# Performance work log

Hardware: AMD Instinct MI355X
Metric: run time of the kernel (lower is better)

## Reference

```python
import jax, jax.numpy as jnp
import numpy as np
import math

B, S, H, DM = 1, 2048, 16, 1024
DK = DM // H
MAX_SEQ = 2048  # rel_embed has MAX_SEQ+1 rows


def setup_inputs() -> dict:
    rng = jax.random.key(0)
    ks = jax.random.split(rng, 12)
    w = lambda k, shape, s=0.02: (jax.random.normal(k, shape, jnp.float32) * s)
    inp = {
        'query': jax.random.normal(ks[0], (B, S, DM), jnp.float32),
        'key':   jax.random.normal(ks[1], (B, S, DM), jnp.float32),
        'value': jax.random.normal(ks[2], (B, S, DM), jnp.float32),
        # causal integer mask [B,S,S] (cumsum over it derives rel-pos indices)
        'mask': jnp.broadcast_to(jnp.tril(jnp.ones((S, S), jnp.int32)), (B, S, S)),
        'Wq': w(ks[3], (DM, DM)), 'bq': jnp.zeros((DM,), jnp.float32),
        'Wk': w(ks[4], (DM, DM)), 'bk': jnp.zeros((DM,), jnp.float32),
        'Wv': w(ks[5], (DM, DM)), 'bv': jnp.zeros((DM,), jnp.float32),
        'Wo': w(ks[6], (DM, DM)), 'bo': jnp.zeros((DM,), jnp.float32),
        # relative position embeddings [h, max_seq_len+1, d_k], N(0,1) as in the module
        'rel_embed': jax.random.normal(ks[7], (H, MAX_SEQ + 1, DK), jnp.float32),
    }
    return inp


def reference(query, key, value, mask, Wq, bq, Wk, bk, Wv, bv, Wo, bo, rel_embed):
    scale = 1.0 / math.sqrt(DK)
    heads = lambda x, W, b: (x @ W.T + b).reshape(B, S, H, DK).transpose(0, 2, 1, 3)
    q = heads(query, Wq, bq)   # [B,H,S,DK]
    k = heads(key, Wk, bk)
    v = heads(value, Wv, bv)

    scores = jnp.einsum('bhid,bhjd->bhij', q, k) * scale  # [B,H,S,S]

    m4 = mask[:, None, :, :]                 # [B,1,S,S]
    nz = m4 != 0
    # torch: cumsum(mask)-1 picks the m-index; index 0 (then zeroed) where mask==0
    m_idx = jnp.where(nz, jnp.cumsum(m4, axis=-1) - 1, 0)  # [B,1,S,S]

    # rel_scores[b,h,m,l] = <q[b,h,l,:], rel_embed[h,m,:]> / sqrt(d_k)
    rel = jnp.einsum('bhld,hmd->bhml', q, rel_embed[:, :S]) * scale  # [B,H,S,S]
    idx = jnp.broadcast_to(m_idx, (B, H, S, S))
    # torch.take flat-index decodes to rel[b,h, m_idx[i,j], j]
    rel_g = jnp.take_along_axis(rel, idx, axis=2) * nz.astype(scores.dtype)

    scores = jnp.where(nz, scores + rel_g, jnp.float32(-1e9))
    p = jax.nn.softmax(scores, axis=-1)      # dropout p=0.0 -> identity

    out = jnp.einsum('bhij,bhjd->bhid', p, v)         # [B,H,S,DK]
    out = out.transpose(0, 2, 1, 3).reshape(B, S, DM)  # [B,S,DM]
    return out @ Wo.T + bo
```

## Files before the change

### kernel.cpp

```cpp
#include <hip/hip_runtime.h>

typedef __bf16 bf16_t;
typedef __bf16 bf16x4 __attribute__((ext_vector_type(4)));
typedef __bf16 bf16x8 __attribute__((ext_vector_type(8)));
typedef float  f32x4  __attribute__((ext_vector_type(4)));
typedef float  f32x16 __attribute__((ext_vector_type(16)));
typedef unsigned int u32;

#define S_LEN 2048
#define DMODEL 1024
#define NHEAD 16
#define DHEAD 64
#define RELROWS 2049

__device__ __forceinline__ void gload16(const void* g, void* l) {
    __builtin_amdgcn_global_load_lds((const __attribute__((address_space(1))) void*)g,
                                     (__attribute__((address_space(3))) void*)l,
                                     16, 0, 0);
}

__device__ __forceinline__ f32x4 mfma16(bf16x8 a, bf16x8 b, f32x4 c) {
    return __builtin_amdgcn_mfma_f32_16x16x32_bf16(a, b, c, 0, 0, 0);
}
__device__ __forceinline__ f32x16 mfma32(bf16x8 a, bf16x8 b, f32x16 c) {
    return __builtin_amdgcn_mfma_f32_32x32x16_bf16(a, b, c, 0, 0, 0);
}

__device__ __forceinline__ bf16x8 lds_read_swz(const bf16_t* base, int row, int colb) {
    return *(const bf16x8*)((const char*)base + row * 128 + (colb ^ ((row & 7) << 4)));
}

__device__ __forceinline__ u32 cvtpk(float lo, float hi) {
    u32 w;
    asm("v_cvt_pk_bf16_f32 %0, %1, %2" : "=v"(w) : "v"(lo), "v"(hi));
    return w;
}
__device__ __forceinline__ void swap32(u32& a, u32& b) {
    asm("v_permlane32_swap_b32 %0, %1" : "+v"(a), "+v"(b));
}
__device__ __forceinline__ float fexp2(float x) {
    float r;
    asm("v_exp_f32 %0, %1" : "=v"(r) : "v"(x));
    return r;
}

__global__ __launch_bounds__(256)
void f2bf_all(const float* __restrict__ xq, const float* __restrict__ xk,
              const float* __restrict__ xv,
              const float* __restrict__ wq, const float* __restrict__ wk,
              const float* __restrict__ wv, const float* __restrict__ wo,
              bf16_t* __restrict__ dst, int n4X, int n4W) {
    const int i = blockIdx.x * blockDim.x + threadIdx.x;
    const float* src; int j;
    if (i < 3 * n4X) {
        if (i < n4X)            { src = xq; j = i; }
        else if (i < 2 * n4X)   { src = xk; j = i - n4X; }
        else                    { src = xv; j = i - 2 * n4X; }
    } else {
        int w = i - 3 * n4X;
        if (w < n4W)            { src = wq; j = w; }
        else if (w < 2 * n4W)   { src = wk; j = w - n4W; }
        else if (w < 3 * n4W)   { src = wv; j = w - 2 * n4W; }
        else                    { src = wo; j = w - 3 * n4W; }
    }
    float4 v = ((const float4*)src)[j];
    bf16x4 o;
    o[0] = (bf16_t)v.x; o[1] = (bf16_t)v.y; o[2] = (bf16_t)v.z; o[3] = (bf16_t)v.w;
    ((bf16x4*)dst)[i] = o;
}

template <int BM, int BN>
__global__ __launch_bounds__(256)
void gemm_qkv(const bf16_t* __restrict__ Abase, const bf16_t* __restrict__ Wbase,
              const float* __restrict__ b0, const float* __restrict__ b1,
              const float* __restrict__ b2,
              bf16_t* __restrict__ outb,
              const float* __restrict__ relp, float* __restrict__ RGout,
              bf16_t* __restrict__ vtp,
              int M, int N, int K) {
    __shared__ alignas(16) bf16_t As[2][BM * 64];
    __shared__ alignas(16) bf16_t Bs[2][BN * 64];
    const int tid = threadIdx.x, lane = tid & 63, wave = tid >> 6;
    const int z = blockIdx.z;
    const bf16_t* A = Abase + (size_t)z * M * K;
    const bf16_t* W = Wbase + (size_t)z * N * K;
    const float* bias = (z == 0) ? b0 : (z == 1 ? b1 : b2);
    const int nwg = gridDim.x * gridDim.y;
    const int wg = blockIdx.y * gridDim.x + blockIdx.x;
    const int swz = (wg & 7) * (nwg >> 3) + (wg >> 3);
    const int m0 = (swz / gridDim.x) * BM, n0 = (swz % gridDim.x) * BN;
    const int wr = (wave >> 1) * (BM / 2), wc = (wave & 1) * (BN / 2);
    constexpr int MR = BM / 32, NR = BN / 32;
    constexpr int LOADS = BM / 32 + BN / 32;

    f32x4 acc[MR][NR] = {};
    const int soff = wave * 1024 + lane * 16;

    auto stage = [&](int b, int kt) {
#pragma unroll
        for (int r = 0; r < BM / 32; ++r) {
            int L = r * 4096 + soff;
            int row = L >> 7, colb = (L & 127) ^ ((row & 7) << 4);
            gload16(A + (size_t)(m0 + row) * K + kt + (colb >> 1),
                    (char*)As[b] + r * 4096 + wave * 1024);
        }
#pragma unroll
        for (int r = 0; r < BN / 32; ++r) {
            int L = r * 4096 + soff;
            int row = L >> 7, colb = (L & 127) ^ ((row & 7) << 4);
            gload16(W + (size_t)(n0 + row) * K + kt + (colb >> 1),
                    (char*)Bs[b] + r * 4096 + wave * 1024);
        }
    };

    const int NK = K >> 6;
    stage(0, 0);
    for (int s = 0; s < NK; ++s) {
        const int buf = s & 1;
        if (s + 1 < NK) {
            stage(buf ^ 1, (s + 1) << 6);
            if constexpr (LOADS == 6) asm volatile("s_waitcnt vmcnt(6)" ::: "memory");
            else if constexpr (LOADS == 4) asm volatile("s_waitcnt vmcnt(4)" ::: "memory");
            else asm volatile("s_waitcnt vmcnt(8)" ::: "memory");
        } else {
            asm volatile("s_waitcnt vmcnt(0)" ::: "memory");
        }
        asm volatile("s_barrier" ::: "memory");
#pragma unroll
        for (int kk = 0; kk < 2; ++kk) {
            bf16x8 af[MR], bfr[NR];
#pragma unroll
            for (int m = 0; m < MR; ++m)
                af[m] = lds_read_swz(As[buf], wr + m * 16 + (lane & 15),
                                     kk * 64 + (lane >> 4) * 16);
#pragma unroll
            for (int n = 0; n < NR; ++n)
                bfr[n] = lds_read_swz(Bs[buf], wc + n * 16 + (lane & 15),
                                      kk * 64 + (lane >> 4) * 16);
#pragma unroll
            for (int m = 0; m < MR; ++m)
#pragma unroll
                for (int n = 0; n < NR; ++n)
                    acc[m][n] = mfma16(af[m], bfr[n], acc[m][n]);
        }
        asm volatile("s_barrier" ::: "memory");
    }

    const float scale = (z == 0) ? 0.18033688011112042f : 1.0f;
    float rp[MR][4];
#pragma unroll
    for (int m = 0; m < MR; ++m)
#pragma unroll
        for (int r2 = 0; r2 < 4; ++r2) rp[m][r2] = 0.f;
    const int hh = n0 >> 6;
#pragma unroll
    for (int m = 0; m < MR; ++m) {
        const int gi = m0 + wr + m * 16 + (lane >> 4) * 4;
#pragma unroll
        for (int n = 0; n < NR; ++n) {
            const int gj = n0 + wc + n * 16 + (lane & 15);
            const float bv = bias[gj];
            if (z == 2) {
                bf16x4 o4;
#pragma unroll
                for (int r2 = 0; r2 < 4; ++r2) o4[r2] = (bf16_t)(acc[m][n][r2] + bv);
                *(bf16x4*)&vtp[(size_t)gj * S_LEN + gi] = o4;
            } else {
#pragma unroll
                for (int r2 = 0; r2 < 4; ++r2) {
                    float v = (acc[m][n][r2] + bv) * scale;
                    outb[(size_t)z * M * N + (size_t)(gi + r2) * N + gj] = (bf16_t)v;
                    if (z == 0)
                        rp[m][r2] += v * relp[((size_t)hh * RELROWS + (gi + r2)) * DHEAD + (gj & 63)];
                }
            }
        }
    }
    if (z == 0) {
        constexpr int HM = BM / 2;
        float* Rp = (float*)As;
#pragma unroll
        for (int m = 0; m < MR; ++m)
#pragma unroll
            for (int r2 = 0; r2 < 4; ++r2) {
                float p = rp[m][r2];
                p += __shfl_xor(p, 1);
                p += __shfl_xor(p, 2);
                p += __shfl_xor(p, 4);
                p += __shfl_xor(p, 8);
                if ((lane & 15) == 0)
                    Rp[wave * HM + m * 16 + (lane >> 4) * 4 + r2] = p;
            }
        __syncthreads();
        if ((wave & 1) == 0) {
#pragma unroll
            for (int rr0 = 0; rr0 < HM; rr0 += 64) {
                int rr = rr0 + lane;
                float v = Rp[wave * HM + rr] + Rp[(wave + 1) * HM + rr];
                RGout[hh * S_LEN + m0 + wr + rr] = v;
            }
        }
    }
}

__global__ __launch_bounds__(256)
void gemm_out(const bf16_t* __restrict__ A, const bf16_t* __restrict__ W,
              const float* __restrict__ bias, float* __restrict__ outf,
              int M, int N, int K) {
    __shared__ alignas(16) bf16_t As[4][64 * 64];
    __shared__ alignas(16) bf16_t Bs[4][64 * 64];
    const int tid = threadIdx.x, lane = tid & 63, wave = tid >> 6;
    const int nwg = gridDim.x * gridDim.y;
    const int wg = blockIdx.y * gridDim.x + blockIdx.x;
    const int swz = (wg & 7) * (nwg >> 3) + (wg >> 3);
    const int m0 = (swz / gridDim.x) * 64, n0 = (swz % gridDim.x) * 64;
    const int wr = (wave >> 1) * 32, wc = (wave & 1) * 32;

    f32x4 acc[2][2] = {};
    const int soff = wave * 1024 + lane * 16;

    auto stage = [&](int b, int kt) {
#pragma unroll
        for (int r = 0; r < 2; ++r) {
            int L = r * 4096 + soff;
            int row = L >> 7, colb = (L & 127) ^ ((row & 7) << 4);
            gload16(A + (size_t)(m0 + row) * K + kt + (colb >> 1),
                    (char*)As[b] + r * 4096 + wave * 1024);
        }
#pragma unroll
        for (int r = 0; r < 2; ++r) {
            int L = r * 4096 + soff;
            int row = L >> 7, colb = (L & 127) ^ ((row & 7) << 4);
            gload16(W + (size_t)(n0 + row) * K + kt + (colb >> 1),
                    (char*)Bs[b] + r * 4096 + wave * 1024);
        }
    };

    const int NK = K >> 6;
    stage(0, 0); stage(1, 64); stage(2, 128);
    for (int s = 0; s < NK; ++s) {
        if (s + 2 < NK)      asm volatile("s_waitcnt vmcnt(8)" ::: "memory");
        else if (s + 1 < NK) asm volatile("s_waitcnt vmcnt(4)" ::: "memory");
        else                 asm volatile("s_waitcnt vmcnt(0)" ::: "memory");
        asm volatile("s_barrier" ::: "memory");
        if (s + 3 < NK) stage((s + 3) & 3, (s + 3) << 6);
        const int buf = s & 3;
#pragma unroll
        for (int kk = 0; kk < 2; ++kk) {
            bf16x8 af[2], bfr[2];
#pragma unroll
            for (int m = 0; m < 2; ++m)
                af[m] = lds_read_swz(As[buf], wr + m * 16 + (lane & 15),
                                     kk * 64 + (lane >> 4) * 16);
#pragma unroll
            for (int n = 0; n < 2; ++n)
                bfr[n] = lds_read_swz(Bs[buf], wc + n * 16 + (lane & 15),
                                      kk * 64 + (lane >> 4) * 16);
#pragma unroll
            for (int m = 0; m < 2; ++m)
#pragma unroll
                for (int n = 0; n < 2; ++n)
                    acc[m][n] = mfma16(af[m], bfr[n], acc[m][n]);
        }
    }
#pragma unroll
    for (int m = 0; m < 2; ++m) {
        const int gi = m0 + wr + m * 16 + (lane >> 4) * 4;
#pragma unroll
        for (int n = 0; n < 2; ++n) {
            const int gj = n0 + wc + n * 16 + (lane & 15);
            const float bv = bias[gj];
#pragma unroll
            for (int r2 = 0; r2 < 4; ++r2)
                outf[(size_t)(gi + r2) * N + gj] = acc[m][n][r2] + bv;
        }
    }
}

__global__ __launch_bounds__(256, 2)
void flash_attn(const bf16_t* __restrict__ Qb, const bf16_t* __restrict__ Kb,
                const bf16_t* __restrict__ Vtp, const float* __restrict__ RG,
                bf16_t* __restrict__ Ob) {
    __shared__ alignas(16) bf16_t KB[4][64 * 64];
    __shared__ alignas(16) bf16_t VB[4][64 * 64];
    __shared__ alignas(16) float Rs[S_LEN];
    const int tid = threadIdx.x, lane = tid & 63, wave = tid >> 6;
    const int h = blockIdx.x;
    const int qt = (int)gridDim.y - 1 - (int)blockIdx.y;
    const int q0 = qt * 32;
    const int nt = (qt >> 1) + 1;
    const int qpar = qt & 1;
    const int lo5 = lane & 31, hi = lane >> 5;

    const int nkv = nt * 64;
    for (int i = tid * 8; i < nkv; i += 2048) {
        *(float4*)&Rs[i]     = *(const float4*)&RG[h * S_LEN + i];
        *(float4*)&Rs[i + 4] = *(const float4*)&RG[h * S_LEN + i + 4];
    }

    const bf16_t* qp = Qb + (size_t)(q0 + lo5) * DMODEL + h * DHEAD;
    bf16x8 qf[4];
#pragma unroll
    for (int c = 0; c < 4; ++c)
        qf[c] = *(const bf16x8*)(qp + c * 16 + hi * 8);

    auto stageK = [&](int tt) {
        char* dst = (char*)KB[wave];
#pragma unroll
        for (int rr = 0; rr < 8; ++rr) {
            int L = rr * 1024 + lane * 16;
            int row = L >> 7, colb = (L & 127) ^ ((row & 7) << 4);
            gload16(Kb + (size_t)(tt * 64 + row) * DMODEL + h * DHEAD + (colb >> 1),
                    dst + rr * 1024);
        }
    };
    auto stageV = [&](int tt) {
        char* dst = (char*)VB[wave];
#pragma unroll
        for (int rr = 0; rr < 8; ++rr) {
            int L = rr * 1024 + lane * 16;
            int row = L >> 7, colb = (L & 127) ^ ((row & 7) << 4);
            gload16(Vtp + (size_t)(h * DHEAD + row) * S_LEN + tt * 64 + (colb >> 1),
                    dst + rr * 1024);
        }
    };

    if (wave < nt) { stageK(wave); stageV(wave); }
    __syncthreads();

    f32x16 oacc[2] = {};
    float ls = 0.f;
    const int thr = qpar * 32 + lo5;

    for (int tt = wave; tt < nt; tt += 4) {
        const int kv0 = tt * 64;
        const bool diag = (tt == nt - 1);
        asm volatile("s_waitcnt vmcnt(8)" ::: "memory");

        f32x16 sta, stb;
#pragma unroll
        for (int g = 0; g < 4; ++g) {
            f32x4 ra = *(const f32x4*)&Rs[kv0 + g * 8 + hi * 4];
            f32x4 rb = *(const f32x4*)&Rs[kv0 + 32 + g * 8 + hi * 4];
#pragma unroll
            for (int e = 0; e < 4; ++e) { sta[g * 4 + e] = ra[e]; stb[g * 4 + e] = rb[e]; }
        }
        __builtin_amdgcn_s_setprio(1);
#pragma unroll
        for (int c = 0; c < 4; ++c) {
            bf16x8 kfa = lds_read_swz(KB[wave], lo5, c * 32 + hi * 16);
            sta = mfma32(kfa, qf[c], sta);
        }
#pragma unroll
        for (int c = 0; c < 4; ++c) {
            bf16x8 kfb = lds_read_swz(KB[wave], 32 + lo5, c * 32 + hi * 16);
            stb = mfma32(kfb, qf[c], stb);
        }
        __builtin_amdgcn_s_setprio(0);
        if (tt + 4 < nt) stageK(tt + 4);

        float pra[16], prb[16];
        if (diag) {
#pragma unroll
            for (int r = 0; r < 16; ++r) {
                int kloc = (r & 3) + 8 * (r >> 2) + 4 * hi;
                float va = fexp2(sta[r]), vb = fexp2(stb[r]);
                pra[r] = (kloc > thr) ? 0.f : va;
                prb[r] = (kloc + 32 > thr) ? 0.f : vb;
            }
        } else {
#pragma unroll
            for (int r = 0; r < 16; ++r) { pra[r] = fexp2(sta[r]); prb[r] = fexp2(stb[r]); }
        }
#pragma unroll
        for (int r = 0; r < 16; ++r) ls += pra[r] + prb[r];
        u32 pw[4][4];
#pragma unroll
        for (int hf = 0; hf < 2; ++hf) {
            u32 a  = cvtpk(pra[8 * hf + 0], pra[8 * hf + 1]);
            u32 b  = cvtpk(pra[8 * hf + 4], pra[8 * hf + 5]);
            swap32(a, b);
            u32 c2 = cvtpk(pra[8 * hf + 2], pra[8 * hf + 3]);
            u32 d2 = cvtpk(pra[8 * hf + 6], pra[8 * hf + 7]);
            swap32(c2, d2);
            pw[hf][0] = a;  pw[hf][1] = c2;  pw[hf][2] = b;  pw[hf][3] = d2;
        }
#pragma unroll
        for (int hf = 0; hf < 2; ++hf) {
            u32 a  = cvtpk(prb[8 * hf + 0], prb[8 * hf + 1]);
            u32 b  = cvtpk(prb[8 * hf + 4], prb[8 * hf + 5]);
            swap32(a, b);
            u32 c2 = cvtpk(prb[8 * hf + 2], prb[8 * hf + 3]);
            u32 d2 = cvtpk(prb[8 * hf + 6], prb[8 * hf + 7]);
            swap32(c2, d2);
            pw[2 + hf][0] = a;  pw[2 + hf][1] = c2;  pw[2 + hf][2] = b;  pw[2 + hf][3] = d2;
        }

        if (tt + 4 < nt) asm volatile("s_waitcnt vmcnt(8)" ::: "memory");
        else             asm volatile("s_waitcnt vmcnt(0)" ::: "memory");

        __builtin_amdgcn_s_setprio(1);
#pragma unroll
        for (int kc = 0; kc < 4; ++kc) {
            union { u32 w[4]; bf16x8 v; } uu;
            uu.w[0] = pw[kc][0]; uu.w[1] = pw[kc][1]; uu.w[2] = pw[kc][2]; uu.w[3] = pw[kc][3];
#pragma unroll
            for (int db = 0; db < 2; ++db) {
                bf16x8 vf = lds_read_swz(VB[wave], db * 32 + lo5, kc * 32 + hi * 16);
                oacc[db] = mfma32(vf, uu.v, oacc[db]);
            }
        }
        __builtin_amdgcn_s_setprio(0);
        if (tt + 4 < nt) stageV(tt + 4);
    }

    asm volatile("s_waitcnt vmcnt(0)" ::: "memory");
    __syncthreads();
    float* scr = (float*)KB;
    if (wave > 0) {
        float* base = scr + (wave - 1) * 2112 + lane * 32;
#pragma unroll
        for (int db = 0; db < 2; ++db)
#pragma unroll
            for (int g = 0; g < 4; ++g) {
                f32x4 v4;
#pragma unroll
                for (int e = 0; e < 4; ++e) v4[e] = oacc[db][g * 4 + e];
                *(f32x4*)(base + db * 16 + g * 4) = v4;
            }
        scr[(wave - 1) * 2112 + 2048 + lane] = ls;
    }
    __syncthreads();
    if (wave == 0) {
#pragma unroll
        for (int w2 = 0; w2 < 3; ++w2) {
            const float* base = scr + w2 * 2112 + lane * 32;
#pragma unroll
            for (int db = 0; db < 2; ++db)
#pragma unroll
                for (int g = 0; g < 4; ++g) {
                    f32x4 v4 = *(const f32x4*)(base + db * 16 + g * 4);
#pragma unroll
                    for (int e = 0; e < 4; ++e) oacc[db][g * 4 + e] += v4[e];
                }
            ls += scr[w2 * 2112 + 2048 + lane];
        }
        ls += __shfl_xor(ls, 32);
        const float inv = 1.0f / ls;
        const int qg = q0 + lo5;
#pragma unroll
        for (int db = 0; db < 2; ++db)
#pragma unroll
            for (int g = 0; g < 4; ++g) {
                bf16x4 o4;
#pragma unroll
                for (int e = 0; e < 4; ++e)
                    o4[e] = (bf16_t)(oacc[db][g * 4 + e] * inv);
                *(bf16x4*)&Ob[(size_t)qg * DMODEL + h * DHEAD + db * 32 + g * 8 + hi * 4] = o4;
            }
    }
}

extern "C" void kernel_launch(void* const* d_in, const int* in_sizes, int n_in,
                              void* d_out, int out_size, void* d_ws, size_t ws_size,
                              hipStream_t stream) {
    const float* query = (const float*)d_in[0];
    const float* key   = (const float*)d_in[1];
    const float* value = (const float*)d_in[2];
    const float* Wq  = (const float*)d_in[4];
    const float* bq  = (const float*)d_in[5];
    const float* Wk  = (const float*)d_in[6];
    const float* bk  = (const float*)d_in[7];
    const float* Wv  = (const float*)d_in[8];
    const float* bv  = (const float*)d_in[9];
    const float* Wo  = (const float*)d_in[10];
    const float* bo  = (const float*)d_in[11];
    const float* rel = (const float*)d_in[12];

    char* ws = (char*)d_ws;
    const size_t nX = (size_t)S_LEN * DMODEL;
    const size_t nW = (size_t)DMODEL * DMODEL;
    bf16_t* Xbf  = (bf16_t*)ws;
    bf16_t* Wbf  = (bf16_t*)(ws + 3 * nX * 2);
    bf16_t* QKV  = (bf16_t*)(ws + 3 * nX * 2 + 4 * nW * 2);
    float*  RG   = (float*)(ws + 3 * nX * 2 + 4 * nW * 2 + 3 * nX * 2);
    bf16_t* Vtp  = QKV + 2 * nX;
    bf16_t* AOb  = (bf16_t*)(ws + nX * 2);
    (void)in_sizes; (void)n_in; (void)out_size; (void)ws_size;

    const int n4X = (int)(nX / 4), n4W = (int)(nW / 4);
    const int tot4 = 3 * n4X + 4 * n4W;
    f2bf_all<<<tot4 / 256, 256, 0, stream>>>(query, key, value, Wq, Wk, Wv, Wo,
                                             Xbf, n4X, n4W);

    gemm_qkv<128, 64><<<dim3(DMODEL / 64, S_LEN / 128, 3), 256, 0, stream>>>(
        Xbf, Wbf, bq, bk, bv, QKV, rel, RG, Vtp, S_LEN, DMODEL, DMODEL);

    flash_attn<<<dim3(NHEAD, S_LEN / 32), 256, 0, stream>>>(QKV, QKV + nX, Vtp, RG, AOb);

    gemm_out<<<dim3(DMODEL / 64, S_LEN / 64), 256, 0, stream>>>(
        AOb, Wbf + 3 * nW, bo, (float*)d_out, S_LEN, DMODEL, DMODEL);
}
```

Measured before the change: 81.34 us.

## Split K across two wave groups in output projection GEMM with LDS reduction

The output projection GEMM now launches 512 threads per block. Two groups of four waves each process half of the K dimension with double buffering instead of a 4-stage pipeline, and the partial accumulators are summed through shared memory before the bias-add store. This is meant to give more waves per tile to hide memory latency and shorten the serial K loop of this small-grid GEMM. In exchange it adds an extra barrier per iteration, an LDS reduction step, and a shallower prefetch pipeline.

```diff
diff --git a/kernel.cpp b/kernel.cpp
--- a/kernel.cpp
+++ b/kernel.cpp
@@ -203,21 +203,23 @@
     }
 }
 
-__global__ __launch_bounds__(256)
+__global__ __launch_bounds__(512)
 void gemm_out(const bf16_t* __restrict__ A, const bf16_t* __restrict__ W,
               const float* __restrict__ bias, float* __restrict__ outf,
               int M, int N, int K) {
-    __shared__ alignas(16) bf16_t As[4][64 * 64];
-    __shared__ alignas(16) bf16_t Bs[4][64 * 64];
+    __shared__ alignas(16) bf16_t As[2][2][64 * 64];
+    __shared__ alignas(16) bf16_t Bs[2][2][64 * 64];
     const int tid = threadIdx.x, lane = tid & 63, wave = tid >> 6;
+    const int grp = wave >> 2, w4 = wave & 3;
     const int nwg = gridDim.x * gridDim.y;
     const int wg = blockIdx.y * gridDim.x + blockIdx.x;
     const int swz = (wg & 7) * (nwg >> 3) + (wg >> 3);
     const int m0 = (swz / gridDim.x) * 64, n0 = (swz % gridDim.x) * 64;
-    const int wr = (wave >> 1) * 32, wc = (wave & 1) * 32;
+    const int wr = (w4 >> 1) * 32, wc = (w4 & 1) * 32;
+    const int kbase = grp * (K >> 1);
 
     f32x4 acc[2][2] = {};
-    const int soff = wave * 1024 + lane * 16;
+    const int soff = w4 * 1024 + lane * 16;
 
     auto stage = [&](int b, int kt) {
 #pragma unroll
@@ -225,36 +227,33 @@
             int L = r * 4096 + soff;
             int row = L >> 7, colb = (L & 127) ^ ((row & 7) << 4);
             gload16(A + (size_t)(m0 + row) * K + kt + (colb >> 1),
-                    (char*)As[b] + r * 4096 + wave * 1024);
-        }
-#pragma unroll
-        for (int r = 0; r < 2; ++r) {
-            int L = r * 4096 + soff;
-            int row = L >> 7, colb = (L & 127) ^ ((row & 7) << 4);
+                    (char*)As[grp][b] + r * 4096 + w4 * 1024);
             gload16(W + (size_t)(n0 + row) * K + kt + (colb >> 1),
-                    (char*)Bs[b] + r * 4096 + wave * 1024);
+                    (char*)Bs[grp][b] + r * 4096 + w4 * 1024);
         }
     };
 
-    const int NK = K >> 6;
-    stage(0, 0); stage(1, 64); stage(2, 128);
-    for (int s = 0; s < NK; ++s) {
-        if (s + 2 < NK)      asm volatile("s_waitcnt vmcnt(8)" ::: "memory");
-        else if (s + 1 < NK) asm volatile("s_waitcnt vmcnt(4)" ::: "memory");
-        else                 asm volatile("s_waitcnt vmcnt(0)" ::: "memory");
+    const int NKg = K >> 7;
+    stage(0, kbase);
+    for (int s = 0; s < NKg; ++s) {
+        const int buf = s & 1;
+        if (s + 1 < NKg) {
+            stage(buf ^ 1, kbase + ((s + 1) << 6));
+            asm volatile("s_waitcnt vmcnt(4)" ::: "memory");
+        } else {
+            asm volatile("s_waitcnt vmcnt(0)" ::: "memory");
+        }
         asm volatile("s_barrier" ::: "memory");
-        if (s + 3 < NK) stage((s + 3) & 3, (s + 3) << 6);
-        const int buf = s & 3;
 #pragma unroll
         for (int kk = 0; kk < 2; ++kk) {
             bf16x8 af[2], bfr[2];
 #pragma unroll
             for (int m = 0; m < 2; ++m)
-                af[m] = lds_read_swz(As[buf], wr + m * 16 + (lane & 15),
+                af[m] = lds_read_swz(As[grp][buf], wr + m * 16 + (lane & 15),
                                      kk * 64 + (lane >> 4) * 16);
 #pragma unroll
             for (int n = 0; n < 2; ++n)
-                bfr[n] = lds_read_swz(Bs[buf], wc + n * 16 + (lane & 15),
+                bfr[n] = lds_read_swz(Bs[grp][buf], wc + n * 16 + (lane & 15),
                                       kk * 64 + (lane >> 4) * 16);
 #pragma unroll
             for (int m = 0; m < 2; ++m)
@@ -262,17 +261,33 @@
                 for (int n = 0; n < 2; ++n)
                     acc[m][n] = mfma16(af[m], bfr[n], acc[m][n]);
         }
-    }
-#pragma unroll
-    for (int m = 0; m < 2; ++m) {
-        const int gi = m0 + wr + m * 16 + (lane >> 4) * 4;
-#pragma unroll
-        for (int n = 0; n < 2; ++n) {
-            const int gj = n0 + wc + n * 16 + (lane & 15);
-            const float bv = bias[gj];
-#pragma unroll
-            for (int r2 = 0; r2 < 4; ++r2)
-                outf[(size_t)(gi + r2) * N + gj] = acc[m][n][r2] + bv;
+        asm volatile("s_barrier" ::: "memory");
+    }
+
+    float* scr = (float*)As;
+    if (grp == 1) {
+        float* base = scr + ((w4 * 64 + lane) << 4);
+#pragma unroll
+        for (int m = 0; m < 2; ++m)
+#pragma unroll
+            for (int n = 0; n < 2; ++n)
+                *(f32x4*)(base + (m * 2 + n) * 4) = acc[m][n];
+    }
+    __syncthreads();
+    if (grp == 0) {
+        const float* base = scr + ((w4 * 64 + lane) << 4);
+#pragma unroll
+        for (int m = 0; m < 2; ++m) {
+            const int gi = m0 + wr + m * 16 + (lane >> 4) * 4;
+#pragma unroll
+            for (int n = 0; n < 2; ++n) {
+                f32x4 ov = *(const f32x4*)(base + (m * 2 + n) * 4);
+                const int gj = n0 + wc + n * 16 + (lane & 15);
+                const float bv = bias[gj];
+#pragma unroll
+                for (int r2 = 0; r2 < 4; ++r2)
+                    outf[(size_t)(gi + r2) * N + gj] = acc[m][n][r2] + ov[r2] + bv;
+            }
         }
     }
 }
@@ -498,6 +513,6 @@
 
     flash_attn<<<dim3(NHEAD, S_LEN / 32), 256, 0, stream>>>(QKV, QKV + nX, Vtp, RG, AOb);
 
-    gemm_out<<<dim3(DMODEL / 64, S_LEN / 64), 256, 0, stream>>>(
+    gemm_out<<<dim3(DMODEL / 64, S_LEN / 64), 512, 0, stream>>>(
         AOb, Wbf + 3 * nW, bo, (float*)d_out, S_LEN, DMODEL, DMODEL);
 }
```

Result: faster. 79.46 us (-2.3%).
